# Optimization experiments

Hardware: AMD Instinct MI355X
Metric: run time of the kernel (lower is better)

Reference implementation:

```python
import jax, jax.numpy as jnp
import numpy as np

T, N = 500, 16384


def setup_inputs() -> dict:
    key = jax.random.key(0)
    k1, k2, k3, k4, k5 = jax.random.split(key, 5)
    z_list = jax.random.normal(k1, (T, N, 2), dtype=jnp.float32) * 10.0
    L_hat_list = jax.random.normal(k2, (T, N, 3), dtype=jnp.float32) * 0.1
    pos0s = jax.random.uniform(k3, (N, 2), dtype=jnp.float32) * 128.0
    vel0s = jax.random.uniform(k4, (N, 2), dtype=jnp.float32) * 2.0 - 1.0
    diag_Q = jax.random.uniform(k5, (4,), dtype=jnp.float32)
    return {"z_list": z_list, "L_hat_list": L_hat_list, "pos0s": pos0s,
            "vel0s": vel0s, "diag_Q": diag_Q, "simplified_cov_update": 1}


def reference(z_list, L_hat_list, pos0s, vel0s, diag_Q, simplified_cov_update):
    dt = z_list.dtype
    n = pos0s.shape[0]
    # Constant-velocity dynamics A, observation matrix Cz (== Cy)
    A = jnp.array([[1., 0., 1., 0.],
                   [0., 1., 0., 1.],
                   [0., 0., 1., 0.],
                   [0., 0., 0., 1.]], dtype=dt)
    Cz = jnp.array([[1., 0., 0., 0.],
                    [0., 1., 0., 0.]], dtype=dt)
    Q = jnp.diag(diag_Q.astype(dt))
    I4 = jnp.eye(4, dtype=dt)

    # pos0s / vel0s provided -> mean0 fully determined, covar0 = I (diag set to 1)
    mean0 = jnp.concatenate([pos0s, vel0s], axis=-1)          # [N, 4]
    covar0 = jnp.broadcast_to(I4, (n, 4, 4)).astype(dt)       # [N, 4, 4]

    def step(carry, inp):
        mean, covar = carry
        z, L_hat = inp
        # ---- predict ----
        mean_pred = mean @ A.T                                    # [N, 4]
        covar_pred = jnp.einsum('ij,njk,lk->nil', A, covar, A) + Q  # [N,4,4]
        # ---- R = L L^T from Cholesky params ----
        l00 = jnp.exp(L_hat[:, 0])
        l10 = L_hat[:, 1]
        l11 = jnp.exp(L_hat[:, 2])
        R = jnp.stack([
            jnp.stack([l00 * l00, l00 * l10], axis=-1),
            jnp.stack([l10 * l00, l10 * l10 + l11 * l11], axis=-1),
        ], axis=-2)                                               # [N, 2, 2]
        # ---- Kalman gain ----
        S = jnp.einsum('ij,njk,lk->nil', Cz, covar_pred, Cz) + R  # [N, 2, 2]
        Sinv = jnp.linalg.inv(S)
        K = jnp.einsum('nij,kj,nkl->nil', covar_pred, Cz, Sinv)   # [N, 4, 2]
        # ---- mean update ----
        innov = z - mean_pred @ Cz.T                              # [N, 2]
        mean_new = mean_pred + jnp.einsum('nij,nj->ni', K, innov)
        # ---- covariance update ----
        IKC = I4 - jnp.einsum('nij,jk->nik', K, Cz)               # [N, 4, 4]
        if simplified_cov_update:
            covar_new = IKC @ covar_pred
        else:
            covar_new = (jnp.einsum('nij,njk,nlk->nil', IKC, covar_pred, IKC)
                         + jnp.einsum('nij,njk,nlk->nil', K, R, K))
        y_hat = mean_new @ Cz.T                                   # Cy == Cz
        return (mean_new, covar_new), y_hat

    (_, _), y_hats = jax.lax.scan(step, (mean0, covar0), (z_list, L_hat_list))
    return y_hats  # [T, N, 2]
```

## Files before the change

kernel.cpp:

```cpp
#include <hip/hip_runtime.h>


#define TSTEPS 500
#define NCHUNK 4
#define MAIN   125
#define WARM   30
#define PF     5
#define LOG2N  14
#define NTRK   16384

struct F3 { float x, y, z; };

__global__ __launch_bounds__(64, 1) void kf_kernel(
    const float* __restrict__ zl,
    const float* __restrict__ lh,
    const float* __restrict__ pos0,
    const float* __restrict__ vel0,
    const float* __restrict__ dq,
    float* __restrict__ yo)
{
    const int tid = threadIdx.x;
    const int n = blockIdx.x * 64 + tid;
    const int chunk = blockIdx.y;
    const int t_store = chunk * MAIN;
    const int t_begin = chunk ? (t_store - WARM) : 0;
    const int t_end = t_store + MAIN;

    const float2* z2 = (const float2*)zl;
    const F3*     l3 = (const F3*)lh;
    float2*       yo2 = (float2*)yo;

    const float q0 = dq[0], q1 = dq[1], q2 = dq[2], q3 = dq[3];

    float m0, m1, m2, m3;
    if (chunk == 0) {
        m0 = pos0[2 * n + 0];
        m1 = pos0[2 * n + 1];
        m2 = vel0[2 * n + 0];
        m3 = vel0[2 * n + 1];
    } else {
        const float2 zz = z2[(t_begin << LOG2N) + n];
        m0 = zz.x; m1 = zz.y; m2 = 0.f; m3 = 0.f;
    }
    float p00 = 1.f, p01 = 0.f, p02 = 0.f, p03 = 0.f;
    float p11 = 1.f, p12 = 0.f, p13 = 0.f;
    float p22 = 1.f, p23 = 0.f;
    float p33 = 1.f;

    float rz0[PF], rz1[PF], rl0[PF], rl1[PF], rl2[PF];
#pragma unroll
    for (int k = 0; k < PF; ++k) {
        const int idx = ((t_begin + k) << LOG2N) + n;
        const float2 zz = z2[idx];
        const F3   ll = l3[idx];
        rz0[k] = zz.x; rz1[k] = zz.y;
        rl0[k] = ll.x; rl1[k] = ll.y; rl2[k] = ll.z;
    }

#define KSTEP(k, tcur, tpre, DO_STORE)                                       \
    {                                                                        \
        const float z0 = rz0[k], z1 = rz1[k];                                \
        const float L0 = rl0[k], L1 = rl1[k], L2 = rl2[k];                   \
        {                            \
            const int idx = ((tpre) << LOG2N) + n;                           \
            const float2 zz = z2[idx];                                       \
            const F3   ll = l3[idx];                                         \
            rz0[k] = zz.x; rz1[k] = zz.y;                                    \
            rl0[k] = ll.x; rl1[k] = ll.y; rl2[k] = ll.z;                     \
        }                                                                    \
                              \
        const float np00 = p00 + p02 + p02 + p22 + q0;                       \
        const float np01 = p01 + p03 + p12 + p23;                            \
        const float np02 = p02 + p22;                                        \
        const float np03 = p03 + p23;                                        \
        const float np11 = p11 + p13 + p13 + p33 + q1;                       \
        const float np12 = p12 + p23;                                        \
        const float np13 = p13 + p33;                                        \
        const float np22 = p22 + q2;                                         \
        const float np23 = p23;                                              \
        const float np33 = p33 + q3;                                         \
        const float m0p = m0 + m2;                                           \
        const float m1p = m1 + m3;                                           \
                                                              \
        const float l00 = __expf(L0);                                        \
        const float l10 = L1;                                                \
        const float l11 = __expf(L2);                                        \
        const float r00 = l00 * l00;                                         \
        const float r01 = l00 * l10;                                         \
        const float r11 = fmaf(l10, l10, l11 * l11);                         \
                               \
        const float s00 = np00 + r00;                                        \
        const float s01 = np01 + r01;                                        \
        const float s11 = np11 + r11;                                        \
        const float det = fmaf(s00, s11, -(s01 * s01));                      \
        const float id  = __builtin_amdgcn_rcpf(det);                        \
        const float i00 = s11 * id;                                          \
        const float i01 = -(s01 * id);                                       \
        const float i11 = s00 * id;                                          \
                                                   \
        const float k00 = fmaf(np00, i00, np01 * i01);                       \
        const float k01 = fmaf(np00, i01, np01 * i11);                       \
        const float k10 = fmaf(np01, i00, np11 * i01);                       \
        const float k11 = fmaf(np01, i01, np11 * i11);                       \
        const float k20 = fmaf(np02, i00, np12 * i01);                       \
        const float k21 = fmaf(np02, i01, np12 * i11);                       \
        const float k30 = fmaf(np03, i00, np13 * i01);                       \
        const float k31 = fmaf(np03, i01, np13 * i11);                       \
                                                            \
        const float e0 = z0 - m0p;                                           \
        const float e1 = z1 - m1p;                                           \
        m0 = fmaf(k01, e1, fmaf(k00, e0, m0p));                              \
        m1 = fmaf(k11, e1, fmaf(k10, e0, m1p));                              \
        m2 = fmaf(k21, e1, fmaf(k20, e0, m2));                               \
        m3 = fmaf(k31, e1, fmaf(k30, e0, m3));                               \
                                   \
        p00 = np00 - fmaf(k00, np00, k01 * np01);                            \
        p01 = np01 - fmaf(k00, np01, k01 * np11);                            \
        p02 = np02 - fmaf(k00, np02, k01 * np12);                            \
        p03 = np03 - fmaf(k00, np03, k01 * np13);                            \
        p11 = np11 - fmaf(k10, np01, k11 * np11);                            \
        p12 = np12 - fmaf(k10, np02, k11 * np12);                            \
        p13 = np13 - fmaf(k10, np03, k11 * np13);                            \
        p22 = np22 - fmaf(k20, np02, k21 * np12);                            \
        p23 = np23 - fmaf(k20, np03, k21 * np13);                            \
        p33 = np33 - fmaf(k30, np03, k31 * np13);                            \
        if (DO_STORE)                                                        \
            yo2[((tcur) << LOG2N) + n] = make_float2(m0, m1);                \
    }

#pragma unroll 1
    for (int tt = t_begin; tt < t_store; tt += PF) {
#pragma unroll
        for (int k = 0; k < PF; ++k) {
            KSTEP(k, tt + k, tt + k + PF, false);
        }
    }

#pragma unroll 1
    for (int tt = t_store; tt < t_end; tt += PF) {
#pragma unroll
        for (int k = 0; k < PF; ++k) {
            int tp = tt + k + PF;
            if (tp > t_end - 1) tp = t_end - 1;
            KSTEP(k, tt + k, tp, true);
        }
    }
#undef KSTEP
}

extern "C" void kernel_launch(void* const* d_in, const int* in_sizes, int n_in,
                              void* d_out, int out_size, void* d_ws, size_t ws_size,
                              hipStream_t stream) {
    const float* zl   = (const float*)d_in[0];
    const float* lh   = (const float*)d_in[1];
    const float* pos0 = (const float*)d_in[2];
    const float* vel0 = (const float*)d_in[3];
    const float* dq   = (const float*)d_in[4];
    float* yo = (float*)d_out;

    dim3 grid(NTRK / 64, NCHUNK);
    kf_kernel<<<grid, 64, 0, stream>>>(zl, lh, pos0, vel0, dq, yo);
}
```

Measured before the change: 44.72 us.

## Process two tracks per thread with packed FP32 and split time into 8 chunks

Each thread now filters two tracks using 2-wide vector types so arithmetic can use packed FP32 instructions. The time axis is split into 8 overlapping chunks with a shorter warmup of 20 steps. This shortens each thread's serial dependency chain and increases instruction-level parallelism. The cost is more warmup overhead per stored step and a possible accuracy loss from the shorter warmup.

```diff
diff --git a/kernel.cpp b/kernel.cpp
--- a/kernel.cpp
+++ b/kernel.cpp
@@ -2,14 +2,18 @@
 
 
 #define TSTEPS 500
-#define NCHUNK 4
-#define MAIN   125
-#define WARM   30
+#define NCHUNK 8
+#define WARM   20
 #define PF     5
 #define LOG2N  14
 #define NTRK   16384
 
+typedef float v2f __attribute__((ext_vector_type(2)));
 struct F3 { float x, y, z; };
+
+__device__ __forceinline__ v2f vfma(v2f a, v2f b, v2f c) {
+    return __builtin_elementwise_fma(a, b, c);
+}
 
 __global__ __launch_bounds__(64, 1) void kf_kernel(
     const float* __restrict__ zl,
@@ -20,11 +24,11 @@
     float* __restrict__ yo)
 {
     const int tid = threadIdx.x;
-    const int n = blockIdx.x * 64 + tid;
-    const int chunk = blockIdx.y;
-    const int t_store = chunk * MAIN;
-    const int t_begin = chunk ? (t_store - WARM) : 0;
-    const int t_end = t_store + MAIN;
+    const int nA = blockIdx.x * 128 + tid;
+    const int c = blockIdx.y;
+    const int t_store = (125 * c) >> 1;
+    const int t_begin = c ? (t_store - WARM) : 0;
+    const bool store_last = (c & 1);
 
     const float2* z2 = (const float2*)zl;
     const F3*     l3 = (const F3*)lh;
@@ -32,119 +36,138 @@
 
     const float q0 = dq[0], q1 = dq[1], q2 = dq[2], q3 = dq[3];
 
-    float m0, m1, m2, m3;
-    if (chunk == 0) {
-        m0 = pos0[2 * n + 0];
-        m1 = pos0[2 * n + 1];
-        m2 = vel0[2 * n + 0];
-        m3 = vel0[2 * n + 1];
+    v2f m0, m1, m2, m3;
+    if (c == 0) {
+        m0 = (v2f){pos0[2 * nA + 0], pos0[2 * (nA + 64) + 0]};
+        m1 = (v2f){pos0[2 * nA + 1], pos0[2 * (nA + 64) + 1]};
+        m2 = (v2f){vel0[2 * nA + 0], vel0[2 * (nA + 64) + 0]};
+        m3 = (v2f){vel0[2 * nA + 1], vel0[2 * (nA + 64) + 1]};
     } else {
-        const float2 zz = z2[(t_begin << LOG2N) + n];
-        m0 = zz.x; m1 = zz.y; m2 = 0.f; m3 = 0.f;
+        const int idx = (t_begin << LOG2N) + nA;
+        const float2 zA = z2[idx];
+        const float2 zB = z2[idx + 64];
+        m0 = (v2f){zA.x, zB.x};
+        m1 = (v2f){zA.y, zB.y};
+        m2 = (v2f){0.f, 0.f};
+        m3 = (v2f){0.f, 0.f};
     }
-    float p00 = 1.f, p01 = 0.f, p02 = 0.f, p03 = 0.f;
-    float p11 = 1.f, p12 = 0.f, p13 = 0.f;
-    float p22 = 1.f, p23 = 0.f;
-    float p33 = 1.f;
+    v2f p00 = {1.f, 1.f}, p01 = {0.f, 0.f}, p02 = {0.f, 0.f}, p03 = {0.f, 0.f};
+    v2f p11 = {1.f, 1.f}, p12 = {0.f, 0.f}, p13 = {0.f, 0.f};
+    v2f p22 = {1.f, 1.f}, p23 = {0.f, 0.f};
+    v2f p33 = {1.f, 1.f};
 
-    float rz0[PF], rz1[PF], rl0[PF], rl1[PF], rl2[PF];
+    v2f rz0[PF], rz1[PF], rl0[PF], rl1[PF], rl2[PF];
 #pragma unroll
     for (int k = 0; k < PF; ++k) {
-        const int idx = ((t_begin + k) << LOG2N) + n;
-        const float2 zz = z2[idx];
-        const F3   ll = l3[idx];
-        rz0[k] = zz.x; rz1[k] = zz.y;
-        rl0[k] = ll.x; rl1[k] = ll.y; rl2[k] = ll.z;
+        const int idx = ((t_begin + k) << LOG2N) + nA;
+        const float2 zA = z2[idx];
+        const float2 zB = z2[idx + 64];
+        const F3 lA = l3[idx];
+        const F3 lB = l3[idx + 64];
+        rz0[k] = (v2f){zA.x, zB.x}; rz1[k] = (v2f){zA.y, zB.y};
+        rl0[k] = (v2f){lA.x, lB.x}; rl1[k] = (v2f){lA.y, lB.y};
+        rl2[k] = (v2f){lA.z, lB.z};
     }
 
-#define KSTEP(k, tcur, tpre, DO_STORE)                                       \
+#define KSTEP(k, tcur, tpre, DO_REFILL, DO_STORE)                            \
     {                                                                        \
-        const float z0 = rz0[k], z1 = rz1[k];                                \
-        const float L0 = rl0[k], L1 = rl1[k], L2 = rl2[k];                   \
-        {                            \
-            const int idx = ((tpre) << LOG2N) + n;                           \
-            const float2 zz = z2[idx];                                       \
-            const F3   ll = l3[idx];                                         \
-            rz0[k] = zz.x; rz1[k] = zz.y;                                    \
-            rl0[k] = ll.x; rl1[k] = ll.y; rl2[k] = ll.z;                     \
+        const v2f z0 = rz0[k], z1 = rz1[k];                                  \
+        const v2f L0 = rl0[k], L1 = rl1[k], L2 = rl2[k];                     \
+        if (DO_REFILL) {                                                     \
+            int tp = (tpre); if (tp > TSTEPS - 1) tp = TSTEPS - 1;           \
+            const int idx = (tp << LOG2N) + nA;                              \
+            const float2 zA = z2[idx];                                       \
+            const float2 zB = z2[idx + 64];                                  \
+            const F3 lA = l3[idx];                                           \
+            const F3 lB = l3[idx + 64];                                      \
+            rz0[k] = (v2f){zA.x, zB.x}; rz1[k] = (v2f){zA.y, zB.y};          \
+            rl0[k] = (v2f){lA.x, lB.x}; rl1[k] = (v2f){lA.y, lB.y};          \
+            rl2[k] = (v2f){lA.z, lB.z};                                      \
         }                                                                    \
                               \
-        const float np00 = p00 + p02 + p02 + p22 + q0;                       \
-        const float np01 = p01 + p03 + p12 + p23;                            \
-        const float np02 = p02 + p22;                                        \
-        const float np03 = p03 + p23;                                        \
-        const float np11 = p11 + p13 + p13 + p33 + q1;                       \
-        const float np12 = p12 + p23;                                        \
-        const float np13 = p13 + p33;                                        \
-        const float np22 = p22 + q2;                                         \
-        const float np23 = p23;                                              \
-        const float np33 = p33 + q3;                                         \
-        const float m0p = m0 + m2;                                           \
-        const float m1p = m1 + m3;                                           \
-                                                              \
-        const float l00 = __expf(L0);                                        \
-        const float l10 = L1;                                                \
-        const float l11 = __expf(L2);                                        \
-        const float r00 = l00 * l00;                                         \
-        const float r01 = l00 * l10;                                         \
-        const float r11 = fmaf(l10, l10, l11 * l11);                         \
+        const v2f np00 = p00 + p02 + p02 + p22 + q0;                         \
+        const v2f np01 = p01 + p03 + p12 + p23;                              \
+        const v2f np02 = p02 + p22;                                          \
+        const v2f np03 = p03 + p23;                                          \
+        const v2f np11 = p11 + p13 + p13 + p33 + q1;                         \
+        const v2f np12 = p12 + p23;                                          \
+        const v2f np13 = p13 + p33;                                          \
+        const v2f np22 = p22 + q2;                                           \
+        const v2f np23 = p23;                                                \
+        const v2f np33 = p33 + q3;                                           \
+        const v2f m0p = m0 + m2;                                             \
+        const v2f m1p = m1 + m3;                                             \
+                   \
+        v2f l00, l11;                                                        \
+        l00.x = __expf(L0.x); l00.y = __expf(L0.y);                          \
+        l11.x = __expf(L2.x); l11.y = __expf(L2.y);                          \
+        const v2f l10 = L1;                                                  \
+        const v2f r00 = l00 * l00;                                           \
+        const v2f r01 = l00 * l10;                                           \
+        const v2f r11 = vfma(l10, l10, l11 * l11);                           \
                                \
-        const float s00 = np00 + r00;                                        \
-        const float s01 = np01 + r01;                                        \
-        const float s11 = np11 + r11;                                        \
-        const float det = fmaf(s00, s11, -(s01 * s01));                      \
-        const float id  = __builtin_amdgcn_rcpf(det);                        \
-        const float i00 = s11 * id;                                          \
-        const float i01 = -(s01 * id);                                       \
-        const float i11 = s00 * id;                                          \
+        const v2f s00 = np00 + r00;                                          \
+        const v2f s01 = np01 + r01;                                          \
+        const v2f s11 = np11 + r11;                                          \
+        const v2f det = vfma(s00, s11, -(s01 * s01));                        \
+        v2f id;                                                              \
+        id.x = __builtin_amdgcn_rcpf(det.x);                                 \
+        id.y = __builtin_amdgcn_rcpf(det.y);                                 \
+        const v2f i00 = s11 * id;                                            \
+        const v2f i01 = -(s01 * id);                                         \
+        const v2f i11 = s00 * id;                                            \
                                                    \
-        const float k00 = fmaf(np00, i00, np01 * i01);                       \
-        const float k01 = fmaf(np00, i01, np01 * i11);                       \
-        const float k10 = fmaf(np01, i00, np11 * i01);                       \
-        const float k11 = fmaf(np01, i01, np11 * i11);                       \
-        const float k20 = fmaf(np02, i00, np12 * i01);                       \
-        const float k21 = fmaf(np02, i01, np12 * i11);                       \
-        const float k30 = fmaf(np03, i00, np13 * i01);                       \
-        const float k31 = fmaf(np03, i01, np13 * i11);                       \
+        const v2f k00 = vfma(np00, i00, np01 * i01);                         \
+        const v2f k01 = vfma(np00, i01, np01 * i11);                         \
+        const v2f k10 = vfma(np01, i00, np11 * i01);                         \
+        const v2f k11 = vfma(np01, i01, np11 * i11);                         \
+        const v2f k20 = vfma(np02, i00, np12 * i01);                         \
+        const v2f k21 = vfma(np02, i01, np12 * i11);                         \
+        const v2f k30 = vfma(np03, i00, np13 * i01);                         \
+        const v2f k31 = vfma(np03, i01, np13 * i11);                         \
                                                             \
-        const float e0 = z0 - m0p;                                           \
-        const float e1 = z1 - m1p;                                           \
-        m0 = fmaf(k01, e1, fmaf(k00, e0, m0p));                              \
-        m1 = fmaf(k11, e1, fmaf(k10, e0, m1p));                              \
-        m2 = fmaf(k21, e1, fmaf(k20, e0, m2));                               \
-        m3 = fmaf(k31, e1, fmaf(k30, e0, m3));                               \
-                                   \
-        p00 = np00 - fmaf(k00, np00, k01 * np01);                            \
-        p01 = np01 - fmaf(k00, np01, k01 * np11);                            \
-        p02 = np02 - fmaf(k00, np02, k01 * np12);                            \
-        p03 = np03 - fmaf(k00, np03, k01 * np13);                            \
-        p11 = np11 - fmaf(k10, np01, k11 * np11);                            \
-        p12 = np12 - fmaf(k10, np02, k11 * np12);                            \
-        p13 = np13 - fmaf(k10, np03, k11 * np13);                            \
-        p22 = np22 - fmaf(k20, np02, k21 * np12);                            \
-        p23 = np23 - fmaf(k20, np03, k21 * np13);                            \
-        p33 = np33 - fmaf(k30, np03, k31 * np13);                            \
-        if (DO_STORE)                                                        \
-            yo2[((tcur) << LOG2N) + n] = make_float2(m0, m1);                \
+        const v2f e0 = z0 - m0p;                                             \
+        const v2f e1 = z1 - m1p;                                             \
+        m0 = vfma(k01, e1, vfma(k00, e0, m0p));                              \
+        m1 = vfma(k11, e1, vfma(k10, e0, m1p));                              \
+        m2 = vfma(k21, e1, vfma(k20, e0, m2));                               \
+        m3 = vfma(k31, e1, vfma(k30, e0, m3));                               \
+                       \
+        p00 = vfma(-k00, np00, vfma(-k01, np01, np00));                      \
+        p01 = vfma(-k00, np01, vfma(-k01, np11, np01));                      \
+        p02 = vfma(-k00, np02, vfma(-k01, np12, np02));                      \
+        p03 = vfma(-k00, np03, vfma(-k01, np13, np03));                      \
+        p11 = vfma(-k10, np01, vfma(-k11, np11, np11));                      \
+        p12 = vfma(-k10, np02, vfma(-k11, np12, np12));                      \
+        p13 = vfma(-k10, np03, vfma(-k11, np13, np13));                      \
+        p22 = vfma(-k20, np02, vfma(-k21, np12, np22));                      \
+        p23 = vfma(-k20, np03, vfma(-k21, np13, np23));                      \
+        p33 = vfma(-k30, np03, vfma(-k31, np13, np33));                      \
+        if (DO_STORE) {                                                      \
+            const int oidx = ((tcur) << LOG2N) + nA;                         \
+            yo2[oidx]      = make_float2(m0.x, m1.x);                        \
+            yo2[oidx + 64] = make_float2(m0.y, m1.y);                        \
+        }                                                                    \
     }
 
 #pragma unroll 1
     for (int tt = t_begin; tt < t_store; tt += PF) {
 #pragma unroll
         for (int k = 0; k < PF; ++k) {
-            KSTEP(k, tt + k, tt + k + PF, false);
+            KSTEP(k, tt + k, tt + k + PF, true, false);
         }
     }
 
 #pragma unroll 1
-    for (int tt = t_store; tt < t_end; tt += PF) {
+    for (int i = 0; i < 60; i += PF) {
 #pragma unroll
         for (int k = 0; k < PF; ++k) {
-            int tp = tt + k + PF;
-            if (tp > t_end - 1) tp = t_end - 1;
-            KSTEP(k, tt + k, tp, true);
+            KSTEP(k, t_store + i + k, t_store + i + k + PF, true, true);
         }
     }
+    KSTEP(0, t_store + 60, 0, false, true);
+    KSTEP(1, t_store + 61, 0, false, true);
+    KSTEP(2, t_store + 62, 0, false, store_last);
 #undef KSTEP
 }
 
@@ -158,6 +181,6 @@
     const float* dq   = (const float*)d_in[4];
     float* yo = (float*)d_out;
 
-    dim3 grid(NTRK / 64, NCHUNK);
+    dim3 grid(NTRK / 128, NCHUNK);
     kf_kernel<<<grid, 64, 0, stream>>>(zl, lh, pos0, vel0, dq, yo);
 }
```

Result: no change. 45.30 us (+1.3%).
